# Optimization experiments

Measured on AMD Instinct MI355X. Metric: run time of the kernel, lower is better.

Reference implementation:

```python
import jax, jax.numpy as jnp
import numpy as np

N = 100000
E = 1600000
F_IN = 32
HID = 16


def _sage_conv(x, src, dst, W_l, b_l, W_r):
    # PyG SAGEConv (aggr='mean', normalize=False, root_weight=True):
    #   out = lin_l(mean_{j in N(i)} x_j) + lin_r(x_i)
    # lin_l has bias, lin_r has no bias.
    n = x.shape[0]
    msg_sum = jax.ops.segment_sum(x[src], dst, num_segments=n)          # [N, d]
    deg = jax.ops.segment_sum(jnp.ones_like(dst, dtype=x.dtype), dst, num_segments=n)
    agg = msg_sum / jnp.maximum(deg, 1.0)[:, None]                      # mean, 0 for isolated nodes
    return agg @ W_l.T + b_l + x @ W_r.T


def setup_inputs() -> dict:
    key = jax.random.key(0)
    ks = jax.random.split(key, 8)
    x = jax.random.normal(ks[0], (N, F_IN), dtype=jnp.float32)
    edge_index = jax.random.randint(ks[1], (1, 2, E), 0, N, dtype=jnp.int64)
    s1 = 1.0 / np.sqrt(F_IN)
    s2 = 1.0 / np.sqrt(HID)
    W1_l = jax.random.uniform(ks[2], (HID, F_IN), jnp.float32, -s1, s1)
    b1_l = jax.random.uniform(ks[3], (HID,), jnp.float32, -s1, s1)
    W1_r = jax.random.uniform(ks[4], (HID, F_IN), jnp.float32, -s1, s1)
    W2_l = jax.random.uniform(ks[5], (F_IN, HID), jnp.float32, -s2, s2)
    b2_l = jax.random.uniform(ks[6], (F_IN,), jnp.float32, -s2, s2)
    W2_r = jax.random.uniform(ks[7], (F_IN, HID), jnp.float32, -s2, s2)
    return {"x": x, "edge_index": edge_index, "W1_l": W1_l, "b1_l": b1_l,
            "W1_r": W1_r, "W2_l": W2_l, "b2_l": b2_l, "W2_r": W2_r}


def reference(x, edge_index, W1_l, b1_l, W1_r, W2_l, b2_l, W2_r):
    ei = jnp.squeeze(edge_index, axis=0)  # [2, E]
    src, dst = ei[0], ei[1]
    h = jax.nn.relu(_sage_conv(x, src, dst, W1_l, b1_l, W1_r))
    out = _sage_conv(h, src, dst, W2_l, b2_l, W2_r)
    return out
```

## Files before the change

kernel.cpp:

```cpp
#include <hip/hip_runtime.h>

#define F_IN 32
#define HID 16
#define BSHIFT 6
#define BNODES (1 << BSHIFT)
#define CAP 1440
#define NBINS 2048
#define CHUNK 8192
#define SRCM 0x1FFFFu
#define WS2 17

__device__ __forceinline__ void add4(float4& a, const float4& b) {
    a.x += b.x; a.y += b.y; a.z += b.z; a.w += b.w;
}
__device__ __forceinline__ unsigned pack2(float a, float b) {
    unsigned ua = __float_as_uint(a);
    unsigned ub = __float_as_uint(b);
    ua = (ua + 0x7FFFu + ((ua >> 16) & 1u)) >> 16;
    ub = (ub + 0x7FFFu + ((ub >> 16) & 1u)) >> 16;
    return ua | (ub << 16);
}
__device__ __forceinline__ float lo2f(unsigned u) { return __uint_as_float(u << 16); }
__device__ __forceinline__ float hi2f(unsigned u) { return __uint_as_float(u & 0xFFFF0000u); }
__device__ __forceinline__ float4 unp(uint2 v) {
    return make_float4(lo2f(v.x), hi2f(v.x), lo2f(v.y), hi2f(v.y));
}

__global__ void __launch_bounds__(256) k_pre(const float* __restrict__ x,
                                             const float* __restrict__ W1_l,
                                             const float* __restrict__ b1,
                                             const float* __restrict__ W1_r,
                                             unsigned* __restrict__ y1b,
                                             float* __restrict__ y1r,
                                             const int* __restrict__ ei,
                                             int* __restrict__ bucketCursor,
                                             unsigned* __restrict__ bucketBuf,
                                             int N, int E, int nodeBlocks) {
    __shared__ int cnt[NBINS];
    __shared__ int runBase[NBINS];
    __shared__ float Wa[HID * F_IN];
    __shared__ float Wb[HID * F_IN];
    __shared__ float bb[HID];
    int tid = threadIdx.x;

    if ((int)blockIdx.x < nodeBlocks) {
        for (int i = tid; i < HID * F_IN; i += 256) { Wa[i] = W1_l[i]; Wb[i] = W1_r[i]; }
        if (tid < HID) bb[tid] = b1[tid];
        __syncthreads();
        int node = blockIdx.x * 256 + tid;
        if (node >= N) return;
        float xr[F_IN];
        const float4* xp = (const float4*)(x + (size_t)node * F_IN);
#pragma unroll
        for (int i = 0; i < F_IN / 4; i++) {
            float4 v = xp[i];
            xr[4 * i + 0] = v.x; xr[4 * i + 1] = v.y;
            xr[4 * i + 2] = v.z; xr[4 * i + 3] = v.w;
        }
        float a[HID];
#pragma unroll
        for (int o = 0; o < HID; o++) {
            float s = 0.f;
#pragma unroll
            for (int k = 0; k < F_IN; k++) s += xr[k] * Wa[o * F_IN + k];
            a[o] = s;
        }
        uint4* yp = (uint4*)(y1b + (size_t)node * 8);
        yp[0] = make_uint4(pack2(a[0], a[1]), pack2(a[2], a[3]),
                           pack2(a[4], a[5]), pack2(a[6], a[7]));
        yp[1] = make_uint4(pack2(a[8], a[9]), pack2(a[10], a[11]),
                           pack2(a[12], a[13]), pack2(a[14], a[15]));
#pragma unroll
        for (int o = 0; o < HID; o++) {
            float s = bb[o];
#pragma unroll
            for (int k = 0; k < F_IN; k++) s += xr[k] * Wb[o * F_IN + k];
            a[o] = s;
        }
        float4* rp = (float4*)(y1r + (size_t)node * HID);
        rp[0] = make_float4(a[0], a[1], a[2], a[3]);
        rp[1] = make_float4(a[4], a[5], a[6], a[7]);
        rp[2] = make_float4(a[8], a[9], a[10], a[11]);
        rp[3] = make_float4(a[12], a[13], a[14], a[15]);
        return;
    }

    int pb = blockIdx.x - nodeBlocks;
    int e0 = pb * CHUNK;
    int e1 = min(e0 + CHUNK, E);
    int n4 = (e1 - e0) >> 2;
    const int4* dst4 = (const int4*)(ei + E + e0);
    const int4* src4 = (const int4*)(ei + e0);

#pragma unroll
    for (int i = 0; i < NBINS / 256; i++) cnt[tid + 256 * i] = 0;
    __syncthreads();
    for (int i = tid; i < n4; i += 256) {
        int4 d = dst4[i];
        atomicAdd(&cnt[d.x >> BSHIFT], 1);
        atomicAdd(&cnt[d.y >> BSHIFT], 1);
        atomicAdd(&cnt[d.z >> BSHIFT], 1);
        atomicAdd(&cnt[d.w >> BSHIFT], 1);
    }
    __syncthreads();
#pragma unroll
    for (int i = 0; i < NBINS / 256; i++) {
        int b = tid + 256 * i;
        int c = cnt[b];
        runBase[b] = c ? atomicAdd(&bucketCursor[b], c) : 0;
        cnt[b] = 0;
    }
    __syncthreads();
    for (int i = tid; i < n4; i += 256) {
        int4 d = dst4[i];
        int4 s = src4[i];
        {
            int b = d.x >> BSHIFT;
            int pos = runBase[b] + atomicAdd(&cnt[b], 1);
            if (pos < CAP)
                bucketBuf[(size_t)b * CAP + pos] = ((unsigned)(d.x & (BNODES - 1)) << 17) | (unsigned)s.x;
        }
        {
            int b = d.y >> BSHIFT;
            int pos = runBase[b] + atomicAdd(&cnt[b], 1);
            if (pos < CAP)
                bucketBuf[(size_t)b * CAP + pos] = ((unsigned)(d.y & (BNODES - 1)) << 17) | (unsigned)s.y;
        }
        {
            int b = d.z >> BSHIFT;
            int pos = runBase[b] + atomicAdd(&cnt[b], 1);
            if (pos < CAP)
                bucketBuf[(size_t)b * CAP + pos] = ((unsigned)(d.z & (BNODES - 1)) << 17) | (unsigned)s.z;
        }
        {
            int b = d.w >> BSHIFT;
            int pos = runBase[b] + atomicAdd(&cnt[b], 1);
            if (pos < CAP)
                bucketBuf[(size_t)b * CAP + pos] = ((unsigned)(d.w & (BNODES - 1)) << 17) | (unsigned)s.w;
        }
    }
}

__global__ void __launch_bounds__(256) k_agg1f(const unsigned* __restrict__ y1b,
                                               const float* __restrict__ y1r,
                                               unsigned* __restrict__ bucketBuf,
                                               const int* __restrict__ bucketCursor,
                                               unsigned* __restrict__ hb,
                                               int* __restrict__ meta, int N) {
    __shared__ __align__(16) unsigned sA[CAP];
    __shared__ __align__(16) unsigned sB[CAP];
    __shared__ int hist[BNODES];
    __shared__ int scn[BNODES];
    __shared__ int cur[BNODES];
    int tid = threadIdx.x, b = blockIdx.x;

    if (tid < BNODES) hist[tid] = 0;
    int nRec = min(bucketCursor[b], CAP);
    unsigned* buf = bucketBuf + (size_t)b * CAP;
    int n4s = (nRec + 3) >> 2;
    for (int i = tid; i < n4s; i += 256)
        ((uint4*)sA)[i] = ((const uint4*)buf)[i];
    __syncthreads();
    for (int i = tid; i < nRec; i += 256) atomicAdd(&hist[sA[i] >> 17], 1);
    __syncthreads();
    if (tid < BNODES) scn[tid] = hist[tid];
    __syncthreads();
    for (int off = 1; off < BNODES; off <<= 1) {
        int v = (tid < BNODES && tid >= off) ? scn[tid - off] : 0;
        __syncthreads();
        if (tid < BNODES && tid >= off) scn[tid] += v;
        __syncthreads();
    }
    if (tid < BNODES) cur[tid] = scn[tid] - hist[tid];
    __syncthreads();
    for (int i = tid; i < nRec; i += 256) {
        unsigned r = sA[i];
        int pos = atomicAdd(&cur[r >> 17], 1);
        sB[pos] = r & SRCM;
    }
    __syncthreads();

    for (int i = tid; i < n4s; i += 256)
        ((uint4*)buf)[i] = ((const uint4*)sB)[i];
    if (tid < BNODES) {
        meta[(size_t)b * 128 + tid] = scn[tid] - hist[tid];
        meta[(size_t)b * 128 + BNODES + tid] = scn[tid];
    }

    const uint2* yv = (const uint2*)y1b;
    {
        int nl = tid >> 2, c = tid & 3;
        int node = b * BNODES + nl;
        if (node < N) {
            int start = scn[nl] - hist[nl];
            int dg = hist[nl];
            int jend = start + dg;
            float4 a0 = make_float4(0, 0, 0, 0), a1 = a0;
            int j = start;
            for (; j + 4 <= jend; j += 4) {
                unsigned s0 = sB[j], s1 = sB[j + 1], s2 = sB[j + 2], s3 = sB[j + 3];
                uint2 v0 = yv[(size_t)s0 * 4 + c];
                uint2 v1 = yv[(size_t)s1 * 4 + c];
                uint2 v2 = yv[(size_t)s2 * 4 + c];
                uint2 v3 = yv[(size_t)s3 * 4 + c];
                add4(a0, unp(v0)); add4(a1, unp(v1));
                add4(a0, unp(v2)); add4(a1, unp(v3));
            }
            for (; j < jend; j++) {
                uint2 v = yv[(size_t)sB[j] * 4 + c];
                add4(a0, unp(v));
            }
            add4(a0, a1);
            float inv = 1.0f / (float)(dg > 0 ? dg : 1);
            float4 r4 = ((const float4*)(y1r + (size_t)node * HID))[c];
            float o0 = fmaxf(a0.x * inv + r4.x, 0.0f);
            float o1 = fmaxf(a0.y * inv + r4.y, 0.0f);
            float o2 = fmaxf(a0.z * inv + r4.z, 0.0f);
            float o3 = fmaxf(a0.w * inv + r4.w, 0.0f);
            ((uint2*)hb)[(size_t)node * 4 + c] = make_uint2(pack2(o0, o1), pack2(o2, o3));
        }
    }
}

__global__ void __launch_bounds__(256) k_l2f(const unsigned* __restrict__ hb,
                                             const unsigned* __restrict__ bucketBuf,
                                             const int* __restrict__ bucketCursor,
                                             const int* __restrict__ meta,
                                             const float* __restrict__ W2_l,
                                             const float* __restrict__ b2,
                                             const float* __restrict__ W2_r,
                                             float* __restrict__ out, int N) {
    __shared__ __align__(16) unsigned sB[CAP];
    __shared__ int s0[BNODES];
    __shared__ int s1[BNODES];
    __shared__ float mm[BNODES * (HID + 1)];
    __shared__ float Wl[F_IN * WS2];
    __shared__ float Wr[F_IN * WS2];
    __shared__ float bs[F_IN];
    int tid = threadIdx.x, b = blockIdx.x;

    for (int i = tid; i < F_IN * HID; i += 256) {
        int r = i >> 4, q = i & 15;
        Wl[r * WS2 + q] = W2_l[i];
        Wr[r * WS2 + q] = W2_r[i];
    }
    if (tid < F_IN) bs[tid] = b2[tid];
    if (tid < BNODES) {
        s0[tid] = meta[(size_t)b * 128 + tid];
        s1[tid] = meta[(size_t)b * 128 + BNODES + tid];
    }
    int nRec = min(bucketCursor[b], CAP);
    const uint4* bv = (const uint4*)(bucketBuf + (size_t)b * CAP);
    int n4s = (nRec + 3) >> 2;
    for (int i = tid; i < n4s; i += 256) ((uint4*)sB)[i] = bv[i];
    __syncthreads();

    const uint2* hv = (const uint2*)hb;
    {
        int nl = tid >> 2, c = tid & 3;
        int node = b * BNODES + nl;
        if (node < N) {
            int start = s0[nl];
            int jend = s1[nl];
            int dg = jend - start;
            float4 a0 = make_float4(0, 0, 0, 0), a1 = a0;
            int j = start;
            for (; j + 4 <= jend; j += 4) {
                unsigned v0i = sB[j], v1i = sB[j + 1], v2i = sB[j + 2], v3i = sB[j + 3];
                uint2 v0 = hv[(size_t)v0i * 4 + c];
                uint2 v1 = hv[(size_t)v1i * 4 + c];
                uint2 v2 = hv[(size_t)v2i * 4 + c];
                uint2 v3 = hv[(size_t)v3i * 4 + c];
                add4(a0, unp(v0)); add4(a1, unp(v1));
                add4(a0, unp(v2)); add4(a1, unp(v3));
            }
            for (; j < jend; j++) {
                uint2 v = hv[(size_t)sB[j] * 4 + c];
                add4(a0, unp(v));
            }
            add4(a0, a1);
            float inv = 1.0f / (float)(dg > 0 ? dg : 1);
            mm[nl * (HID + 1) + c * 4 + 0] = a0.x * inv;
            mm[nl * (HID + 1) + c * 4 + 1] = a0.y * inv;
            mm[nl * (HID + 1) + c * 4 + 2] = a0.z * inv;
            mm[nl * (HID + 1) + c * 4 + 3] = a0.w * inv;
        }
    }
    __syncthreads();

    {
        int nl = tid >> 2, c = tid & 3;
        int node = b * BNODES + nl;
        if (node >= N) return;

        float m[HID];
#pragma unroll
        for (int k = 0; k < HID; k++) m[k] = mm[nl * (HID + 1) + k];

        float hr[HID];
        const uint4* hp = (const uint4*)(hb + (size_t)node * 8);
        uint4 u0 = hp[0], u1 = hp[1];
        hr[0] = lo2f(u0.x); hr[1] = hi2f(u0.x); hr[2] = lo2f(u0.y); hr[3] = hi2f(u0.y);
        hr[4] = lo2f(u0.z); hr[5] = hi2f(u0.z); hr[6] = lo2f(u0.w); hr[7] = hi2f(u0.w);
        hr[8] = lo2f(u1.x); hr[9] = hi2f(u1.x); hr[10] = lo2f(u1.y); hr[11] = hi2f(u1.y);
        hr[12] = lo2f(u1.z); hr[13] = hi2f(u1.z); hr[14] = lo2f(u1.w); hr[15] = hi2f(u1.w);

        float a[8];
#pragma unroll
        for (int jj = 0; jj < 8; jj++) {
            int o = c * 8 + jj;
            float s = bs[o];
#pragma unroll
            for (int k = 0; k < HID; k++)
                s += m[k] * Wl[o * WS2 + k] + hr[k] * Wr[o * WS2 + k];
            a[jj] = s;
        }
        float4* op = (float4*)(out + (size_t)node * F_IN + c * 8);
        op[0] = make_float4(a[0], a[1], a[2], a[3]);
        op[1] = make_float4(a[4], a[5], a[6], a[7]);
    }
}

extern "C" void kernel_launch(void* const* d_in, const int* in_sizes, int n_in,
                              void* d_out, int out_size, void* d_ws, size_t ws_size,
                              hipStream_t stream) {
    const float* x    = (const float*)d_in[0];
    const int*   ei   = (const int*)d_in[1];
    const float* W1_l = (const float*)d_in[2];
    const float* b1   = (const float*)d_in[3];
    const float* W1_r = (const float*)d_in[4];
    const float* W2_l = (const float*)d_in[5];
    const float* b2   = (const float*)d_in[6];
    const float* W2_r = (const float*)d_in[7];
    float* out = (float*)d_out;

    const int N = in_sizes[0] / F_IN;
    const int E = in_sizes[1] / 2;
    const int nbuckets = (N + BNODES - 1) >> BSHIFT;

    int* bucketCursor = (int*)d_ws;
    unsigned* bucketBuf = (unsigned*)(bucketCursor + NBINS);
    unsigned* y1b = bucketBuf + (size_t)nbuckets * CAP;
    unsigned* hb  = y1b + (size_t)N * 8;
    int* meta = (int*)(hb + (size_t)N * 8);
    float* y1r = (float*)(meta + (size_t)nbuckets * 128);

    hipMemsetAsync(bucketCursor, 0, NBINS * sizeof(int), stream);

    const int nodeBlocks = (N + 255) / 256;
    const int partBlocks = (E + CHUNK - 1) / CHUNK;

    k_pre<<<nodeBlocks + partBlocks, 256, 0, stream>>>(x, W1_l, b1, W1_r,
                                                       y1b, y1r, ei,
                                                       bucketCursor, bucketBuf,
                                                       N, E, nodeBlocks);
    k_agg1f<<<nbuckets, 256, 0, stream>>>(y1b, y1r, bucketBuf, bucketCursor,
                                          hb, meta, N);
    k_l2f<<<nbuckets, 256, 0, stream>>>(hb, bucketBuf, bucketCursor, meta,
                                        W2_l, b2, W2_r, out, N);
}
```

Before: 147.3 us.

## Replace bucket binning with per-node fixed-capacity adjacency via global atomics

Drops the two-level bucket partition (shared-memory histogram, bucket cursors, then an in-block counting sort in the first aggregation kernel). Each edge now does a global atomicAdd on its destination's degree and writes its source straight into a fixed 64-slot per-node adjacency row. The aggregation kernels then read neighbour lists directly from that row with vectorised loads, so the per-bucket sort and the meta array are gone. In exchange there are 1.6M contended global atomics, scattered 4-byte writes, a larger memset of the degree array, and silently truncated neighbour lists for any node with more than 64 in-edges.

```diff
diff --git a/kernel.cpp b/kernel.cpp
--- a/kernel.cpp
+++ b/kernel.cpp
@@ -2,12 +2,9 @@
 
 #define F_IN 32
 #define HID 16
-#define BSHIFT 6
-#define BNODES (1 << BSHIFT)
-#define CAP 1440
-#define NBINS 2048
-#define CHUNK 8192
-#define SRCM 0x1FFFFu
+#define CAPN 64
+#define CSH 6
+#define CHUNK 4096
 #define WS2 17
 
 __device__ __forceinline__ void add4(float4& a, const float4& b) {
@@ -33,17 +30,15 @@
                                              unsigned* __restrict__ y1b,
                                              float* __restrict__ y1r,
                                              const int* __restrict__ ei,
-                                             int* __restrict__ bucketCursor,
-                                             unsigned* __restrict__ bucketBuf,
+                                             int* __restrict__ deg,
+                                             unsigned* __restrict__ csr,
                                              int N, int E, int nodeBlocks) {
-    __shared__ int cnt[NBINS];
-    __shared__ int runBase[NBINS];
-    __shared__ float Wa[HID * F_IN];
-    __shared__ float Wb[HID * F_IN];
-    __shared__ float bb[HID];
     int tid = threadIdx.x;
 
     if ((int)blockIdx.x < nodeBlocks) {
+        __shared__ float Wa[HID * F_IN];
+        __shared__ float Wb[HID * F_IN];
+        __shared__ float bb[HID];
         for (int i = tid; i < HID * F_IN; i += 256) { Wa[i] = W1_l[i]; Wb[i] = W1_r[i]; }
         if (tid < HID) bb[tid] = b1[tid];
         __syncthreads();
@@ -92,152 +87,72 @@
     const int4* dst4 = (const int4*)(ei + E + e0);
     const int4* src4 = (const int4*)(ei + e0);
 
-#pragma unroll
-    for (int i = 0; i < NBINS / 256; i++) cnt[tid + 256 * i] = 0;
-    __syncthreads();
-    for (int i = tid; i < n4; i += 256) {
-        int4 d = dst4[i];
-        atomicAdd(&cnt[d.x >> BSHIFT], 1);
-        atomicAdd(&cnt[d.y >> BSHIFT], 1);
-        atomicAdd(&cnt[d.z >> BSHIFT], 1);
-        atomicAdd(&cnt[d.w >> BSHIFT], 1);
-    }
-    __syncthreads();
-#pragma unroll
-    for (int i = 0; i < NBINS / 256; i++) {
-        int b = tid + 256 * i;
-        int c = cnt[b];
-        runBase[b] = c ? atomicAdd(&bucketCursor[b], c) : 0;
-        cnt[b] = 0;
-    }
-    __syncthreads();
     for (int i = tid; i < n4; i += 256) {
         int4 d = dst4[i];
         int4 s = src4[i];
-        {
-            int b = d.x >> BSHIFT;
-            int pos = runBase[b] + atomicAdd(&cnt[b], 1);
-            if (pos < CAP)
-                bucketBuf[(size_t)b * CAP + pos] = ((unsigned)(d.x & (BNODES - 1)) << 17) | (unsigned)s.x;
-        }
-        {
-            int b = d.y >> BSHIFT;
-            int pos = runBase[b] + atomicAdd(&cnt[b], 1);
-            if (pos < CAP)
-                bucketBuf[(size_t)b * CAP + pos] = ((unsigned)(d.y & (BNODES - 1)) << 17) | (unsigned)s.y;
-        }
-        {
-            int b = d.z >> BSHIFT;
-            int pos = runBase[b] + atomicAdd(&cnt[b], 1);
-            if (pos < CAP)
-                bucketBuf[(size_t)b * CAP + pos] = ((unsigned)(d.z & (BNODES - 1)) << 17) | (unsigned)s.z;
-        }
-        {
-            int b = d.w >> BSHIFT;
-            int pos = runBase[b] + atomicAdd(&cnt[b], 1);
-            if (pos < CAP)
-                bucketBuf[(size_t)b * CAP + pos] = ((unsigned)(d.w & (BNODES - 1)) << 17) | (unsigned)s.w;
-        }
-    }
-}
-
-__global__ void __launch_bounds__(256) k_agg1f(const unsigned* __restrict__ y1b,
-                                               const float* __restrict__ y1r,
-                                               unsigned* __restrict__ bucketBuf,
-                                               const int* __restrict__ bucketCursor,
-                                               unsigned* __restrict__ hb,
-                                               int* __restrict__ meta, int N) {
-    __shared__ __align__(16) unsigned sA[CAP];
-    __shared__ __align__(16) unsigned sB[CAP];
-    __shared__ int hist[BNODES];
-    __shared__ int scn[BNODES];
-    __shared__ int cur[BNODES];
-    int tid = threadIdx.x, b = blockIdx.x;
-
-    if (tid < BNODES) hist[tid] = 0;
-    int nRec = min(bucketCursor[b], CAP);
-    unsigned* buf = bucketBuf + (size_t)b * CAP;
-    int n4s = (nRec + 3) >> 2;
-    for (int i = tid; i < n4s; i += 256)
-        ((uint4*)sA)[i] = ((const uint4*)buf)[i];
-    __syncthreads();
-    for (int i = tid; i < nRec; i += 256) atomicAdd(&hist[sA[i] >> 17], 1);
-    __syncthreads();
-    if (tid < BNODES) scn[tid] = hist[tid];
-    __syncthreads();
-    for (int off = 1; off < BNODES; off <<= 1) {
-        int v = (tid < BNODES && tid >= off) ? scn[tid - off] : 0;
-        __syncthreads();
-        if (tid < BNODES && tid >= off) scn[tid] += v;
-        __syncthreads();
-    }
-    if (tid < BNODES) cur[tid] = scn[tid] - hist[tid];
-    __syncthreads();
-    for (int i = tid; i < nRec; i += 256) {
-        unsigned r = sA[i];
-        int pos = atomicAdd(&cur[r >> 17], 1);
-        sB[pos] = r & SRCM;
-    }
-    __syncthreads();
-
-    for (int i = tid; i < n4s; i += 256)
-        ((uint4*)buf)[i] = ((const uint4*)sB)[i];
-    if (tid < BNODES) {
-        meta[(size_t)b * 128 + tid] = scn[tid] - hist[tid];
-        meta[(size_t)b * 128 + BNODES + tid] = scn[tid];
-    }
-
+        int p0 = atomicAdd(&deg[d.x], 1);
+        int p1 = atomicAdd(&deg[d.y], 1);
+        int p2 = atomicAdd(&deg[d.z], 1);
+        int p3 = atomicAdd(&deg[d.w], 1);
+        if (p0 < CAPN) csr[((size_t)d.x << CSH) | p0] = (unsigned)s.x;
+        if (p1 < CAPN) csr[((size_t)d.y << CSH) | p1] = (unsigned)s.y;
+        if (p2 < CAPN) csr[((size_t)d.z << CSH) | p2] = (unsigned)s.z;
+        if (p3 < CAPN) csr[((size_t)d.w << CSH) | p3] = (unsigned)s.w;
+    }
+}
+
+__global__ void __launch_bounds__(256) k_agg1(const unsigned* __restrict__ y1b,
+                                              const float* __restrict__ y1r,
+                                              const unsigned* __restrict__ csr,
+                                              const int* __restrict__ deg,
+                                              unsigned* __restrict__ hb, int N) {
+    int tid = threadIdx.x;
+    int nl = tid >> 2, c = tid & 3;
+    int node = blockIdx.x * 64 + nl;
+    if (node >= N) return;
+    int dg = deg[node];
+    int cnt = min(dg, CAPN);
+    const unsigned* cp = csr + ((size_t)node << CSH);
     const uint2* yv = (const uint2*)y1b;
-    {
-        int nl = tid >> 2, c = tid & 3;
-        int node = b * BNODES + nl;
-        if (node < N) {
-            int start = scn[nl] - hist[nl];
-            int dg = hist[nl];
-            int jend = start + dg;
-            float4 a0 = make_float4(0, 0, 0, 0), a1 = a0;
-            int j = start;
-            for (; j + 4 <= jend; j += 4) {
-                unsigned s0 = sB[j], s1 = sB[j + 1], s2 = sB[j + 2], s3 = sB[j + 3];
-                uint2 v0 = yv[(size_t)s0 * 4 + c];
-                uint2 v1 = yv[(size_t)s1 * 4 + c];
-                uint2 v2 = yv[(size_t)s2 * 4 + c];
-                uint2 v3 = yv[(size_t)s3 * 4 + c];
-                add4(a0, unp(v0)); add4(a1, unp(v1));
-                add4(a0, unp(v2)); add4(a1, unp(v3));
-            }
-            for (; j < jend; j++) {
-                uint2 v = yv[(size_t)sB[j] * 4 + c];
-                add4(a0, unp(v));
-            }
-            add4(a0, a1);
-            float inv = 1.0f / (float)(dg > 0 ? dg : 1);
-            float4 r4 = ((const float4*)(y1r + (size_t)node * HID))[c];
-            float o0 = fmaxf(a0.x * inv + r4.x, 0.0f);
-            float o1 = fmaxf(a0.y * inv + r4.y, 0.0f);
-            float o2 = fmaxf(a0.z * inv + r4.z, 0.0f);
-            float o3 = fmaxf(a0.w * inv + r4.w, 0.0f);
-            ((uint2*)hb)[(size_t)node * 4 + c] = make_uint2(pack2(o0, o1), pack2(o2, o3));
-        }
-    }
-}
-
-__global__ void __launch_bounds__(256) k_l2f(const unsigned* __restrict__ hb,
-                                             const unsigned* __restrict__ bucketBuf,
-                                             const int* __restrict__ bucketCursor,
-                                             const int* __restrict__ meta,
-                                             const float* __restrict__ W2_l,
-                                             const float* __restrict__ b2,
-                                             const float* __restrict__ W2_r,
-                                             float* __restrict__ out, int N) {
-    __shared__ __align__(16) unsigned sB[CAP];
-    __shared__ int s0[BNODES];
-    __shared__ int s1[BNODES];
-    __shared__ float mm[BNODES * (HID + 1)];
+    float4 a0 = make_float4(0, 0, 0, 0), a1 = a0;
+    int j = 0;
+    for (; j + 4 <= cnt; j += 4) {
+        uint4 sv = *(const uint4*)(cp + j);
+        uint2 v0 = yv[(size_t)sv.x * 4 + c];
+        uint2 v1 = yv[(size_t)sv.y * 4 + c];
+        uint2 v2 = yv[(size_t)sv.z * 4 + c];
+        uint2 v3 = yv[(size_t)sv.w * 4 + c];
+        add4(a0, unp(v0)); add4(a1, unp(v1));
+        add4(a0, unp(v2)); add4(a1, unp(v3));
+    }
+    for (; j < cnt; j++) {
+        uint2 v = yv[(size_t)cp[j] * 4 + c];
+        add4(a0, unp(v));
+    }
+    add4(a0, a1);
+    float inv = 1.0f / (float)(dg > 0 ? dg : 1);
+    float4 r4 = ((const float4*)(y1r + (size_t)node * HID))[c];
+    float o0 = fmaxf(a0.x * inv + r4.x, 0.0f);
+    float o1 = fmaxf(a0.y * inv + r4.y, 0.0f);
+    float o2 = fmaxf(a0.z * inv + r4.z, 0.0f);
+    float o3 = fmaxf(a0.w * inv + r4.w, 0.0f);
+    ((uint2*)hb)[(size_t)node * 4 + c] = make_uint2(pack2(o0, o1), pack2(o2, o3));
+}
+
+__global__ void __launch_bounds__(256) k_l2(const unsigned* __restrict__ hb,
+                                            const unsigned* __restrict__ csr,
+                                            const int* __restrict__ deg,
+                                            const float* __restrict__ W2_l,
+                                            const float* __restrict__ b2,
+                                            const float* __restrict__ W2_r,
+                                            float* __restrict__ out, int N) {
+    __shared__ float mm[64 * (HID + 1)];
     __shared__ float Wl[F_IN * WS2];
     __shared__ float Wr[F_IN * WS2];
     __shared__ float bs[F_IN];
-    int tid = threadIdx.x, b = blockIdx.x;
+    int tid = threadIdx.x;
+    int nl = tid >> 2, c = tid & 3;
+    int node = blockIdx.x * 64 + nl;
 
     for (int i = tid; i < F_IN * HID; i += 256) {
         int r = i >> 4, q = i & 15;
@@ -245,80 +160,63 @@
         Wr[r * WS2 + q] = W2_r[i];
     }
     if (tid < F_IN) bs[tid] = b2[tid];
-    if (tid < BNODES) {
-        s0[tid] = meta[(size_t)b * 128 + tid];
-        s1[tid] = meta[(size_t)b * 128 + BNODES + tid];
-    }
-    int nRec = min(bucketCursor[b], CAP);
-    const uint4* bv = (const uint4*)(bucketBuf + (size_t)b * CAP);
-    int n4s = (nRec + 3) >> 2;
-    for (int i = tid; i < n4s; i += 256) ((uint4*)sB)[i] = bv[i];
+
+    if (node < N) {
+        int dg = deg[node];
+        int cnt = min(dg, CAPN);
+        const unsigned* cp = csr + ((size_t)node << CSH);
+        const uint2* hv = (const uint2*)hb;
+        float4 a0 = make_float4(0, 0, 0, 0), a1 = a0;
+        int j = 0;
+        for (; j + 4 <= cnt; j += 4) {
+            uint4 sv = *(const uint4*)(cp + j);
+            uint2 v0 = hv[(size_t)sv.x * 4 + c];
+            uint2 v1 = hv[(size_t)sv.y * 4 + c];
+            uint2 v2 = hv[(size_t)sv.z * 4 + c];
+            uint2 v3 = hv[(size_t)sv.w * 4 + c];
+            add4(a0, unp(v0)); add4(a1, unp(v1));
+            add4(a0, unp(v2)); add4(a1, unp(v3));
+        }
+        for (; j < cnt; j++) {
+            uint2 v = hv[(size_t)cp[j] * 4 + c];
+            add4(a0, unp(v));
+        }
+        add4(a0, a1);
+        float inv = 1.0f / (float)(dg > 0 ? dg : 1);
+        mm[nl * (HID + 1) + c * 4 + 0] = a0.x * inv;
+        mm[nl * (HID + 1) + c * 4 + 1] = a0.y * inv;
+        mm[nl * (HID + 1) + c * 4 + 2] = a0.z * inv;
+        mm[nl * (HID + 1) + c * 4 + 3] = a0.w * inv;
+    }
     __syncthreads();
 
-    const uint2* hv = (const uint2*)hb;
-    {
-        int nl = tid >> 2, c = tid & 3;
-        int node = b * BNODES + nl;
-        if (node < N) {
-            int start = s0[nl];
-            int jend = s1[nl];
-            int dg = jend - start;
-            float4 a0 = make_float4(0, 0, 0, 0), a1 = a0;
-            int j = start;
-            for (; j + 4 <= jend; j += 4) {
-                unsigned v0i = sB[j], v1i = sB[j + 1], v2i = sB[j + 2], v3i = sB[j + 3];
-                uint2 v0 = hv[(size_t)v0i * 4 + c];
-                uint2 v1 = hv[(size_t)v1i * 4 + c];
-                uint2 v2 = hv[(size_t)v2i * 4 + c];
-                uint2 v3 = hv[(size_t)v3i * 4 + c];
-                add4(a0, unp(v0)); add4(a1, unp(v1));
-                add4(a0, unp(v2)); add4(a1, unp(v3));
-            }
-            for (; j < jend; j++) {
-                uint2 v = hv[(size_t)sB[j] * 4 + c];
-                add4(a0, unp(v));
-            }
-            add4(a0, a1);
-            float inv = 1.0f / (float)(dg > 0 ? dg : 1);
-            mm[nl * (HID + 1) + c * 4 + 0] = a0.x * inv;
-            mm[nl * (HID + 1) + c * 4 + 1] = a0.y * inv;
-            mm[nl * (HID + 1) + c * 4 + 2] = a0.z * inv;
-            mm[nl * (HID + 1) + c * 4 + 3] = a0.w * inv;
-        }
-    }
-    __syncthreads();
-
-    {
-        int nl = tid >> 2, c = tid & 3;
-        int node = b * BNODES + nl;
-        if (node >= N) return;
-
-        float m[HID];
-#pragma unroll
-        for (int k = 0; k < HID; k++) m[k] = mm[nl * (HID + 1) + k];
-
-        float hr[HID];
-        const uint4* hp = (const uint4*)(hb + (size_t)node * 8);
-        uint4 u0 = hp[0], u1 = hp[1];
-        hr[0] = lo2f(u0.x); hr[1] = hi2f(u0.x); hr[2] = lo2f(u0.y); hr[3] = hi2f(u0.y);
-        hr[4] = lo2f(u0.z); hr[5] = hi2f(u0.z); hr[6] = lo2f(u0.w); hr[7] = hi2f(u0.w);
-        hr[8] = lo2f(u1.x); hr[9] = hi2f(u1.x); hr[10] = lo2f(u1.y); hr[11] = hi2f(u1.y);
-        hr[12] = lo2f(u1.z); hr[13] = hi2f(u1.z); hr[14] = lo2f(u1.w); hr[15] = hi2f(u1.w);
-
-        float a[8];
-#pragma unroll
-        for (int jj = 0; jj < 8; jj++) {
-            int o = c * 8 + jj;
-            float s = bs[o];
-#pragma unroll
-            for (int k = 0; k < HID; k++)
-                s += m[k] * Wl[o * WS2 + k] + hr[k] * Wr[o * WS2 + k];
-            a[jj] = s;
-        }
-        float4* op = (float4*)(out + (size_t)node * F_IN + c * 8);
-        op[0] = make_float4(a[0], a[1], a[2], a[3]);
-        op[1] = make_float4(a[4], a[5], a[6], a[7]);
-    }
+    if (node >= N) return;
+
+    float m[HID];
+#pragma unroll
+    for (int k = 0; k < HID; k++) m[k] = mm[nl * (HID + 1) + k];
+
+    float hr[HID];
+    const uint4* hp = (const uint4*)(hb + (size_t)node * 8);
+    uint4 u0 = hp[0], u1 = hp[1];
+    hr[0] = lo2f(u0.x); hr[1] = hi2f(u0.x); hr[2] = lo2f(u0.y); hr[3] = hi2f(u0.y);
+    hr[4] = lo2f(u0.z); hr[5] = hi2f(u0.z); hr[6] = lo2f(u0.w); hr[7] = hi2f(u0.w);
+    hr[8] = lo2f(u1.x); hr[9] = hi2f(u1.x); hr[10] = lo2f(u1.y); hr[11] = hi2f(u1.y);
+    hr[12] = lo2f(u1.z); hr[13] = hi2f(u1.z); hr[14] = lo2f(u1.w); hr[15] = hi2f(u1.w);
+
+    float a[8];
+#pragma unroll
+    for (int jj = 0; jj < 8; jj++) {
+        int o = c * 8 + jj;
+        float s = bs[o];
+#pragma unroll
+        for (int k = 0; k < HID; k++)
+            s += m[k] * Wl[o * WS2 + k] + hr[k] * Wr[o * WS2 + k];
+        a[jj] = s;
+    }
+    float4* op = (float4*)(out + (size_t)node * F_IN + c * 8);
+    op[0] = make_float4(a[0], a[1], a[2], a[3]);
+    op[1] = make_float4(a[4], a[5], a[6], a[7]);
 }
 
 extern "C" void kernel_launch(void* const* d_in, const int* in_sizes, int n_in,
@@ -336,26 +234,23 @@
 
     const int N = in_sizes[0] / F_IN;
     const int E = in_sizes[1] / 2;
-    const int nbuckets = (N + BNODES - 1) >> BSHIFT;
-
-    int* bucketCursor = (int*)d_ws;
-    unsigned* bucketBuf = (unsigned*)(bucketCursor + NBINS);
-    unsigned* y1b = bucketBuf + (size_t)nbuckets * CAP;
+    const int Npad = (N + 1023) & ~1023;
+
+    int* deg = (int*)d_ws;
+    unsigned* csr = (unsigned*)(deg + Npad);
+    unsigned* y1b = csr + ((size_t)N << CSH);
     unsigned* hb  = y1b + (size_t)N * 8;
-    int* meta = (int*)(hb + (size_t)N * 8);
-    float* y1r = (float*)(meta + (size_t)nbuckets * 128);
-
-    hipMemsetAsync(bucketCursor, 0, NBINS * sizeof(int), stream);
+    float* y1r = (float*)(hb + (size_t)N * 8);
+
+    hipMemsetAsync(deg, 0, Npad * sizeof(int), stream);
 
     const int nodeBlocks = (N + 255) / 256;
     const int partBlocks = (E + CHUNK - 1) / CHUNK;
+    const int aggBlocks  = (N + 63) / 64;
 
     k_pre<<<nodeBlocks + partBlocks, 256, 0, stream>>>(x, W1_l, b1, W1_r,
                                                        y1b, y1r, ei,
-                                                       bucketCursor, bucketBuf,
-                                                       N, E, nodeBlocks);
-    k_agg1f<<<nbuckets, 256, 0, stream>>>(y1b, y1r, bucketBuf, bucketCursor,
-                                          hb, meta, N);
-    k_l2f<<<nbuckets, 256, 0, stream>>>(hb, bucketBuf, bucketCursor, meta,
-                                        W2_l, b2, W2_r, out, N);
-}
+                                                       deg, csr, N, E, nodeBlocks);
+    k_agg1<<<aggBlocks, 256, 0, stream>>>(y1b, y1r, csr, deg, hb, N);
+    k_l2<<<aggBlocks, 256, 0, stream>>>(hb, csr, deg, W2_l, b2, W2_r, out, N);
+}
```

Measured after the change: 231.5 us. 1.57x slower.

## Fuse three kernels into one persistent kernel with software grid barriers

Applied to the files above, without the earlier changes.

Merges the preprocessing/partition, layer-1 aggregation and layer-2 kernels into a single persistent kernel of 768 blocks. Blocks loop over jobs and buckets and are separated by atomic-counter grid barriers. This removes two kernel launch gaps and the tail effects between stages. In exchange, each barrier spins on a global atomic. The fixed grid must be fully co-resident for the barriers to work, otherwise the kernel deadlocks, and the grid-stride loops reduce per-stage parallelism compared with the original launches.

```diff
diff --git a/kernel.cpp b/kernel.cpp
--- a/kernel.cpp
+++ b/kernel.cpp
@@ -9,6 +9,9 @@
 #define CHUNK 8192
 #define SRCM 0x1FFFFu
 #define WS2 17
+#define GRIDN 768
+
+#define SMEM_BYTES 16384
 
 __device__ __forceinline__ void add4(float4& a, const float4& b) {
     a.x += b.x; a.y += b.y; a.z += b.z; a.w += b.w;
@@ -26,298 +29,302 @@
     return make_float4(lo2f(v.x), hi2f(v.x), lo2f(v.y), hi2f(v.y));
 }
 
-__global__ void __launch_bounds__(256) k_pre(const float* __restrict__ x,
-                                             const float* __restrict__ W1_l,
-                                             const float* __restrict__ b1,
-                                             const float* __restrict__ W1_r,
-                                             unsigned* __restrict__ y1b,
-                                             float* __restrict__ y1r,
-                                             const int* __restrict__ ei,
-                                             int* __restrict__ bucketCursor,
-                                             unsigned* __restrict__ bucketBuf,
-                                             int N, int E, int nodeBlocks) {
-    __shared__ int cnt[NBINS];
-    __shared__ int runBase[NBINS];
-    __shared__ float Wa[HID * F_IN];
-    __shared__ float Wb[HID * F_IN];
-    __shared__ float bb[HID];
-    int tid = threadIdx.x;
-
-    if ((int)blockIdx.x < nodeBlocks) {
-        for (int i = tid; i < HID * F_IN; i += 256) { Wa[i] = W1_l[i]; Wb[i] = W1_r[i]; }
-        if (tid < HID) bb[tid] = b1[tid];
-        __syncthreads();
-        int node = blockIdx.x * 256 + tid;
-        if (node >= N) return;
-        float xr[F_IN];
-        const float4* xp = (const float4*)(x + (size_t)node * F_IN);
-#pragma unroll
-        for (int i = 0; i < F_IN / 4; i++) {
-            float4 v = xp[i];
-            xr[4 * i + 0] = v.x; xr[4 * i + 1] = v.y;
-            xr[4 * i + 2] = v.z; xr[4 * i + 3] = v.w;
-        }
-        float a[HID];
-#pragma unroll
-        for (int o = 0; o < HID; o++) {
-            float s = 0.f;
-#pragma unroll
-            for (int k = 0; k < F_IN; k++) s += xr[k] * Wa[o * F_IN + k];
-            a[o] = s;
-        }
-        uint4* yp = (uint4*)(y1b + (size_t)node * 8);
-        yp[0] = make_uint4(pack2(a[0], a[1]), pack2(a[2], a[3]),
-                           pack2(a[4], a[5]), pack2(a[6], a[7]));
-        yp[1] = make_uint4(pack2(a[8], a[9]), pack2(a[10], a[11]),
-                           pack2(a[12], a[13]), pack2(a[14], a[15]));
-#pragma unroll
-        for (int o = 0; o < HID; o++) {
-            float s = bb[o];
-#pragma unroll
-            for (int k = 0; k < F_IN; k++) s += xr[k] * Wb[o * F_IN + k];
-            a[o] = s;
-        }
-        float4* rp = (float4*)(y1r + (size_t)node * HID);
-        rp[0] = make_float4(a[0], a[1], a[2], a[3]);
-        rp[1] = make_float4(a[4], a[5], a[6], a[7]);
-        rp[2] = make_float4(a[8], a[9], a[10], a[11]);
-        rp[3] = make_float4(a[12], a[13], a[14], a[15]);
-        return;
-    }
-
-    int pb = blockIdx.x - nodeBlocks;
-    int e0 = pb * CHUNK;
-    int e1 = min(e0 + CHUNK, E);
-    int n4 = (e1 - e0) >> 2;
-    const int4* dst4 = (const int4*)(ei + E + e0);
-    const int4* src4 = (const int4*)(ei + e0);
-
-#pragma unroll
-    for (int i = 0; i < NBINS / 256; i++) cnt[tid + 256 * i] = 0;
+__device__ __forceinline__ void gbar(int* cnt, int target) {
+    __threadfence();
     __syncthreads();
-    for (int i = tid; i < n4; i += 256) {
-        int4 d = dst4[i];
-        atomicAdd(&cnt[d.x >> BSHIFT], 1);
-        atomicAdd(&cnt[d.y >> BSHIFT], 1);
-        atomicAdd(&cnt[d.z >> BSHIFT], 1);
-        atomicAdd(&cnt[d.w >> BSHIFT], 1);
+    if (threadIdx.x == 0) {
+        atomicAdd(cnt, 1);
+        while (__hip_atomic_load(cnt, __ATOMIC_RELAXED, __HIP_MEMORY_SCOPE_AGENT) < target)
+            __builtin_amdgcn_s_sleep(32);
     }
     __syncthreads();
-#pragma unroll
-    for (int i = 0; i < NBINS / 256; i++) {
-        int b = tid + 256 * i;
-        int c = cnt[b];
-        runBase[b] = c ? atomicAdd(&bucketCursor[b], c) : 0;
-        cnt[b] = 0;
+    __threadfence();
+}
+
+__global__ void __launch_bounds__(256, 4)
+k_mega(const float* __restrict__ x, const float* __restrict__ W1_l,
+       const float* __restrict__ b1, const float* __restrict__ W1_r,
+       const float* __restrict__ W2_l, const float* __restrict__ b2,
+       const float* __restrict__ W2_r, const int* __restrict__ ei,
+       int* __restrict__ gsync, int* __restrict__ bucketCursor,
+       unsigned* __restrict__ bucketBuf, unsigned* __restrict__ y1b,
+       float* __restrict__ y1r, unsigned* __restrict__ hb,
+       int* __restrict__ meta, float* __restrict__ out,
+       int N, int E, int nodeBlocks, int partBlocks, int nbuckets) {
+    __shared__ __align__(16) unsigned char smem[SMEM_BYTES];
+    int tid = threadIdx.x;
+    int bid = blockIdx.x;
+    int nG = gridDim.x;
+
+    for (int job = bid; job < nodeBlocks + partBlocks; job += nG) {
+        if (job < nodeBlocks) {
+            float* Wa = (float*)smem;
+            float* Wb = (float*)(smem + 2048);
+            float* bb = (float*)(smem + 4096);
+            for (int i = tid; i < HID * F_IN; i += 256) { Wa[i] = W1_l[i]; Wb[i] = W1_r[i]; }
+            if (tid < HID) bb[tid] = b1[tid];
+            __syncthreads();
+            int node = job * 256 + tid;
+            if (node < N) {
+                float xr[F_IN];
+                const float4* xp = (const float4*)(x + (size_t)node * F_IN);
+#pragma unroll
+                for (int i = 0; i < F_IN / 4; i++) {
+                    float4 v = xp[i];
+                    xr[4 * i + 0] = v.x; xr[4 * i + 1] = v.y;
+                    xr[4 * i + 2] = v.z; xr[4 * i + 3] = v.w;
+                }
+                float a[HID];
+#pragma unroll
+                for (int o = 0; o < HID; o++) {
+                    float s = 0.f;
+#pragma unroll
+                    for (int k = 0; k < F_IN; k++) s += xr[k] * Wa[o * F_IN + k];
+                    a[o] = s;
+                }
+                uint4* yp = (uint4*)(y1b + (size_t)node * 8);
+                yp[0] = make_uint4(pack2(a[0], a[1]), pack2(a[2], a[3]),
+                                   pack2(a[4], a[5]), pack2(a[6], a[7]));
+                yp[1] = make_uint4(pack2(a[8], a[9]), pack2(a[10], a[11]),
+                                   pack2(a[12], a[13]), pack2(a[14], a[15]));
+#pragma unroll
+                for (int o = 0; o < HID; o++) {
+                    float s = bb[o];
+#pragma unroll
+                    for (int k = 0; k < F_IN; k++) s += xr[k] * Wb[o * F_IN + k];
+                    a[o] = s;
+                }
+                float4* rp = (float4*)(y1r + (size_t)node * HID);
+                rp[0] = make_float4(a[0], a[1], a[2], a[3]);
+                rp[1] = make_float4(a[4], a[5], a[6], a[7]);
+                rp[2] = make_float4(a[8], a[9], a[10], a[11]);
+                rp[3] = make_float4(a[12], a[13], a[14], a[15]);
+            }
+        } else {
+            int* cnt = (int*)smem;
+            int* runBase = (int*)(smem + 8192);
+            int pb = job - nodeBlocks;
+            int e0 = pb * CHUNK;
+            int e1 = min(e0 + CHUNK, E);
+            int n4 = (e1 - e0) >> 2;
+            const int4* dst4 = (const int4*)(ei + E + e0);
+            const int4* src4 = (const int4*)(ei + e0);
+
+#pragma unroll
+            for (int i = 0; i < NBINS / 256; i++) cnt[tid + 256 * i] = 0;
+            __syncthreads();
+            for (int i = tid; i < n4; i += 256) {
+                int4 d = dst4[i];
+                atomicAdd(&cnt[d.x >> BSHIFT], 1);
+                atomicAdd(&cnt[d.y >> BSHIFT], 1);
+                atomicAdd(&cnt[d.z >> BSHIFT], 1);
+                atomicAdd(&cnt[d.w >> BSHIFT], 1);
+            }
+            __syncthreads();
+#pragma unroll
+            for (int i = 0; i < NBINS / 256; i++) {
+                int b = tid + 256 * i;
+                int c = cnt[b];
+                runBase[b] = c ? atomicAdd(&bucketCursor[b], c) : 0;
+                cnt[b] = 0;
+            }
+            __syncthreads();
+            for (int i = tid; i < n4; i += 256) {
+                int4 d = dst4[i];
+                int4 s = src4[i];
+                {
+                    int b = d.x >> BSHIFT;
+                    int pos = runBase[b] + atomicAdd(&cnt[b], 1);
+                    if (pos < CAP)
+                        bucketBuf[(size_t)b * CAP + pos] = ((unsigned)(d.x & (BNODES - 1)) << 17) | (unsigned)s.x;
+                }
+                {
+                    int b = d.y >> BSHIFT;
+                    int pos = runBase[b] + atomicAdd(&cnt[b], 1);
+                    if (pos < CAP)
+                        bucketBuf[(size_t)b * CAP + pos] = ((unsigned)(d.y & (BNODES - 1)) << 17) | (unsigned)s.y;
+                }
+                {
+                    int b = d.z >> BSHIFT;
+                    int pos = runBase[b] + atomicAdd(&cnt[b], 1);
+                    if (pos < CAP)
+                        bucketBuf[(size_t)b * CAP + pos] = ((unsigned)(d.z & (BNODES - 1)) << 17) | (unsigned)s.z;
+                }
+                {
+                    int b = d.w >> BSHIFT;
+                    int pos = runBase[b] + atomicAdd(&cnt[b], 1);
+                    if (pos < CAP)
+                        bucketBuf[(size_t)b * CAP + pos] = ((unsigned)(d.w & (BNODES - 1)) << 17) | (unsigned)s.w;
+                }
+            }
+        }
+        __syncthreads();
     }
-    __syncthreads();
-    for (int i = tid; i < n4; i += 256) {
-        int4 d = dst4[i];
-        int4 s = src4[i];
-        {
-            int b = d.x >> BSHIFT;
-            int pos = runBase[b] + atomicAdd(&cnt[b], 1);
-            if (pos < CAP)
-                bucketBuf[(size_t)b * CAP + pos] = ((unsigned)(d.x & (BNODES - 1)) << 17) | (unsigned)s.x;
-        }
-        {
-            int b = d.y >> BSHIFT;
-            int pos = runBase[b] + atomicAdd(&cnt[b], 1);
-            if (pos < CAP)
-                bucketBuf[(size_t)b * CAP + pos] = ((unsigned)(d.y & (BNODES - 1)) << 17) | (unsigned)s.y;
-        }
-        {
-            int b = d.z >> BSHIFT;
-            int pos = runBase[b] + atomicAdd(&cnt[b], 1);
-            if (pos < CAP)
-                bucketBuf[(size_t)b * CAP + pos] = ((unsigned)(d.z & (BNODES - 1)) << 17) | (unsigned)s.z;
-        }
-        {
-            int b = d.w >> BSHIFT;
-            int pos = runBase[b] + atomicAdd(&cnt[b], 1);
-            if (pos < CAP)
-                bucketBuf[(size_t)b * CAP + pos] = ((unsigned)(d.w & (BNODES - 1)) << 17) | (unsigned)s.w;
+    gbar(gsync, nG);
+
+    {
+        unsigned* sA = (unsigned*)smem;
+        unsigned* sB = (unsigned*)(smem + 5760);
+        int* hist = (int*)(smem + 11520);
+        int* scn  = (int*)(smem + 11776);
+        int* cur  = (int*)(smem + 12032);
+        for (int b = bid; b < nbuckets; b += nG) {
+            if (tid < BNODES) hist[tid] = 0;
+            int nRec = min(bucketCursor[b], CAP);
+            unsigned* buf = bucketBuf + (size_t)b * CAP;
+            int n4s = (nRec + 3) >> 2;
+            for (int i = tid; i < n4s; i += 256)
+                ((uint4*)sA)[i] = ((const uint4*)buf)[i];
+            __syncthreads();
+            for (int i = tid; i < nRec; i += 256) atomicAdd(&hist[sA[i] >> 17], 1);
+            __syncthreads();
+            if (tid < BNODES) scn[tid] = hist[tid];
+            __syncthreads();
+            for (int off = 1; off < BNODES; off <<= 1) {
+                int v = (tid < BNODES && tid >= off) ? scn[tid - off] : 0;
+                __syncthreads();
+                if (tid < BNODES && tid >= off) scn[tid] += v;
+                __syncthreads();
+            }
+            if (tid < BNODES) cur[tid] = scn[tid] - hist[tid];
+            __syncthreads();
+            for (int i = tid; i < nRec; i += 256) {
+                unsigned r = sA[i];
+                int pos = atomicAdd(&cur[r >> 17], 1);
+                sB[pos] = r & SRCM;
+            }
+            __syncthreads();
+
+            for (int i = tid; i < n4s; i += 256)
+                ((uint4*)buf)[i] = ((const uint4*)sB)[i];
+            if (tid < BNODES) {
+                meta[(size_t)b * 128 + tid] = scn[tid] - hist[tid];
+                meta[(size_t)b * 128 + BNODES + tid] = scn[tid];
+            }
+
+            const uint2* yv = (const uint2*)y1b;
+            {
+                int nl = tid >> 2, c = tid & 3;
+                int node = b * BNODES + nl;
+                if (node < N) {
+                    int start = scn[nl] - hist[nl];
+                    int dg = hist[nl];
+                    int jend = start + dg;
+                    float4 a0 = make_float4(0, 0, 0, 0), a1 = a0;
+                    int j = start;
+                    for (; j + 4 <= jend; j += 4) {
+                        unsigned s0 = sB[j], s1 = sB[j + 1], s2 = sB[j + 2], s3 = sB[j + 3];
+                        uint2 v0 = yv[(size_t)s0 * 4 + c];
+                        uint2 v1 = yv[(size_t)s1 * 4 + c];
+                        uint2 v2 = yv[(size_t)s2 * 4 + c];
+                        uint2 v3 = yv[(size_t)s3 * 4 + c];
+                        add4(a0, unp(v0)); add4(a1, unp(v1));
+                        add4(a0, unp(v2)); add4(a1, unp(v3));
+                    }
+                    for (; j < jend; j++) {
+                        uint2 v = yv[(size_t)sB[j] * 4 + c];
+                        add4(a0, unp(v));
+                    }
+                    add4(a0, a1);
+                    float inv = 1.0f / (float)(dg > 0 ? dg : 1);
+                    float4 r4 = ((const float4*)(y1r + (size_t)node * HID))[c];
+                    float o0 = fmaxf(a0.x * inv + r4.x, 0.0f);
+                    float o1 = fmaxf(a0.y * inv + r4.y, 0.0f);
+                    float o2 = fmaxf(a0.z * inv + r4.z, 0.0f);
+                    float o3 = fmaxf(a0.w * inv + r4.w, 0.0f);
+                    ((uint2*)hb)[(size_t)node * 4 + c] = make_uint2(pack2(o0, o1), pack2(o2, o3));
+                }
+            }
+            __syncthreads();
         }
     }
-}
-
-__global__ void __launch_bounds__(256) k_agg1f(const unsigned* __restrict__ y1b,
-                                               const float* __restrict__ y1r,
-                                               unsigned* __restrict__ bucketBuf,
-                                               const int* __restrict__ bucketCursor,
-                                               unsigned* __restrict__ hb,
-                                               int* __restrict__ meta, int N) {
-    __shared__ __align__(16) unsigned sA[CAP];
-    __shared__ __align__(16) unsigned sB[CAP];
-    __shared__ int hist[BNODES];
-    __shared__ int scn[BNODES];
-    __shared__ int cur[BNODES];
-    int tid = threadIdx.x, b = blockIdx.x;
-
-    if (tid < BNODES) hist[tid] = 0;
-    int nRec = min(bucketCursor[b], CAP);
-    unsigned* buf = bucketBuf + (size_t)b * CAP;
-    int n4s = (nRec + 3) >> 2;
-    for (int i = tid; i < n4s; i += 256)
-        ((uint4*)sA)[i] = ((const uint4*)buf)[i];
-    __syncthreads();
-    for (int i = tid; i < nRec; i += 256) atomicAdd(&hist[sA[i] >> 17], 1);
-    __syncthreads();
-    if (tid < BNODES) scn[tid] = hist[tid];
-    __syncthreads();
-    for (int off = 1; off < BNODES; off <<= 1) {
-        int v = (tid < BNODES && tid >= off) ? scn[tid - off] : 0;
-        __syncthreads();
-        if (tid < BNODES && tid >= off) scn[tid] += v;
-        __syncthreads();
-    }
-    if (tid < BNODES) cur[tid] = scn[tid] - hist[tid];
-    __syncthreads();
-    for (int i = tid; i < nRec; i += 256) {
-        unsigned r = sA[i];
-        int pos = atomicAdd(&cur[r >> 17], 1);
-        sB[pos] = r & SRCM;
-    }
-    __syncthreads();
-
-    for (int i = tid; i < n4s; i += 256)
-        ((uint4*)buf)[i] = ((const uint4*)sB)[i];
-    if (tid < BNODES) {
-        meta[(size_t)b * 128 + tid] = scn[tid] - hist[tid];
-        meta[(size_t)b * 128 + BNODES + tid] = scn[tid];
-    }
-
-    const uint2* yv = (const uint2*)y1b;
+    gbar(gsync, 2 * nG);
+
     {
-        int nl = tid >> 2, c = tid & 3;
-        int node = b * BNODES + nl;
-        if (node < N) {
-            int start = scn[nl] - hist[nl];
-            int dg = hist[nl];
-            int jend = start + dg;
-            float4 a0 = make_float4(0, 0, 0, 0), a1 = a0;
-            int j = start;
-            for (; j + 4 <= jend; j += 4) {
-                unsigned s0 = sB[j], s1 = sB[j + 1], s2 = sB[j + 2], s3 = sB[j + 3];
-                uint2 v0 = yv[(size_t)s0 * 4 + c];
-                uint2 v1 = yv[(size_t)s1 * 4 + c];
-                uint2 v2 = yv[(size_t)s2 * 4 + c];
-                uint2 v3 = yv[(size_t)s3 * 4 + c];
-                add4(a0, unp(v0)); add4(a1, unp(v1));
-                add4(a0, unp(v2)); add4(a1, unp(v3));
-            }
-            for (; j < jend; j++) {
-                uint2 v = yv[(size_t)sB[j] * 4 + c];
-                add4(a0, unp(v));
-            }
-            add4(a0, a1);
-            float inv = 1.0f / (float)(dg > 0 ? dg : 1);
-            float4 r4 = ((const float4*)(y1r + (size_t)node * HID))[c];
-            float o0 = fmaxf(a0.x * inv + r4.x, 0.0f);
-            float o1 = fmaxf(a0.y * inv + r4.y, 0.0f);
-            float o2 = fmaxf(a0.z * inv + r4.z, 0.0f);
-            float o3 = fmaxf(a0.w * inv + r4.w, 0.0f);
-            ((uint2*)hb)[(size_t)node * 4 + c] = make_uint2(pack2(o0, o1), pack2(o2, o3));
+        unsigned* sL = (unsigned*)smem;
+        int* s0a = (int*)(smem + 5760);
+        int* s1a = (int*)(smem + 6016);
+        float* mm = (float*)(smem + 6272);
+        float* Wl = (float*)(smem + 10624);
+        float* Wr = (float*)(smem + 12800);
+        float* bs = (float*)(smem + 14976);
+        for (int i = tid; i < F_IN * HID; i += 256) {
+            int r = i >> 4, q = i & 15;
+            Wl[r * WS2 + q] = W2_l[i];
+            Wr[r * WS2 + q] = W2_r[i];
         }
-    }
-}
-
-__global__ void __launch_bounds__(256) k_l2f(const unsigned* __restrict__ hb,
-                                             const unsigned* __restrict__ bucketBuf,
-                                             const int* __restrict__ bucketCursor,
-                                             const int* __restrict__ meta,
-                                             const float* __restrict__ W2_l,
-                                             const float* __restrict__ b2,
-                                             const float* __restrict__ W2_r,
-                                             float* __restrict__ out, int N) {
-    __shared__ __align__(16) unsigned sB[CAP];
-    __shared__ int s0[BNODES];
-    __shared__ int s1[BNODES];
-    __shared__ float mm[BNODES * (HID + 1)];
-    __shared__ float Wl[F_IN * WS2];
-    __shared__ float Wr[F_IN * WS2];
-    __shared__ float bs[F_IN];
-    int tid = threadIdx.x, b = blockIdx.x;
-
-    for (int i = tid; i < F_IN * HID; i += 256) {
-        int r = i >> 4, q = i & 15;
-        Wl[r * WS2 + q] = W2_l[i];
-        Wr[r * WS2 + q] = W2_r[i];
-    }
-    if (tid < F_IN) bs[tid] = b2[tid];
-    if (tid < BNODES) {
-        s0[tid] = meta[(size_t)b * 128 + tid];
-        s1[tid] = meta[(size_t)b * 128 + BNODES + tid];
-    }
-    int nRec = min(bucketCursor[b], CAP);
-    const uint4* bv = (const uint4*)(bucketBuf + (size_t)b * CAP);
-    int n4s = (nRec + 3) >> 2;
-    for (int i = tid; i < n4s; i += 256) ((uint4*)sB)[i] = bv[i];
-    __syncthreads();
-
-    const uint2* hv = (const uint2*)hb;
-    {
-        int nl = tid >> 2, c = tid & 3;
-        int node = b * BNODES + nl;
-        if (node < N) {
-            int start = s0[nl];
-            int jend = s1[nl];
-            int dg = jend - start;
-            float4 a0 = make_float4(0, 0, 0, 0), a1 = a0;
-            int j = start;
-            for (; j + 4 <= jend; j += 4) {
-                unsigned v0i = sB[j], v1i = sB[j + 1], v2i = sB[j + 2], v3i = sB[j + 3];
-                uint2 v0 = hv[(size_t)v0i * 4 + c];
-                uint2 v1 = hv[(size_t)v1i * 4 + c];
-                uint2 v2 = hv[(size_t)v2i * 4 + c];
-                uint2 v3 = hv[(size_t)v3i * 4 + c];
-                add4(a0, unp(v0)); add4(a1, unp(v1));
-                add4(a0, unp(v2)); add4(a1, unp(v3));
-            }
-            for (; j < jend; j++) {
-                uint2 v = hv[(size_t)sB[j] * 4 + c];
-                add4(a0, unp(v));
-            }
-            add4(a0, a1);
-            float inv = 1.0f / (float)(dg > 0 ? dg : 1);
-            mm[nl * (HID + 1) + c * 4 + 0] = a0.x * inv;
-            mm[nl * (HID + 1) + c * 4 + 1] = a0.y * inv;
-            mm[nl * (HID + 1) + c * 4 + 2] = a0.z * inv;
-            mm[nl * (HID + 1) + c * 4 + 3] = a0.w * inv;
+        if (tid < F_IN) bs[tid] = b2[tid];
+        for (int b = bid; b < nbuckets; b += nG) {
+            if (tid < BNODES) {
+                s0a[tid] = meta[(size_t)b * 128 + tid];
+                s1a[tid] = meta[(size_t)b * 128 + BNODES + tid];
+            }
+            int nRec = min(bucketCursor[b], CAP);
+            const uint4* bv = (const uint4*)(bucketBuf + (size_t)b * CAP);
+            int n4s = (nRec + 3) >> 2;
+            for (int i = tid; i < n4s; i += 256) ((uint4*)sL)[i] = bv[i];
+            __syncthreads();
+
+            int nl = tid >> 2, c = tid & 3;
+            int node = b * BNODES + nl;
+            const uint2* hv = (const uint2*)hb;
+            if (node < N) {
+                int start = s0a[nl];
+                int jend = s1a[nl];
+                int dg = jend - start;
+                float4 a0 = make_float4(0, 0, 0, 0), a1 = a0;
+                int j = start;
+                for (; j + 4 <= jend; j += 4) {
+                    unsigned v0i = sL[j], v1i = sL[j + 1], v2i = sL[j + 2], v3i = sL[j + 3];
+                    uint2 v0 = hv[(size_t)v0i * 4 + c];
+                    uint2 v1 = hv[(size_t)v1i * 4 + c];
+                    uint2 v2 = hv[(size_t)v2i * 4 + c];
+                    uint2 v3 = hv[(size_t)v3i * 4 + c];
+                    add4(a0, unp(v0)); add4(a1, unp(v1));
+                    add4(a0, unp(v2)); add4(a1, unp(v3));
+                }
+                for (; j < jend; j++) {
+                    uint2 v = hv[(size_t)sL[j] * 4 + c];
+                    add4(a0, unp(v));
+                }
+                add4(a0, a1);
+                float inv = 1.0f / (float)(dg > 0 ? dg : 1);
+                mm[nl * (HID + 1) + c * 4 + 0] = a0.x * inv;
+                mm[nl * (HID + 1) + c * 4 + 1] = a0.y * inv;
+                mm[nl * (HID + 1) + c * 4 + 2] = a0.z * inv;
+                mm[nl * (HID + 1) + c * 4 + 3] = a0.w * inv;
+            }
+            __syncthreads();
+
+            if (node < N) {
+                float m[HID];
+#pragma unroll
+                for (int k = 0; k < HID; k++) m[k] = mm[nl * (HID + 1) + k];
+
+                float hr[HID];
+                const uint4* hp = (const uint4*)(hb + (size_t)node * 8);
+                uint4 u0 = hp[0], u1 = hp[1];
+                hr[0] = lo2f(u0.x); hr[1] = hi2f(u0.x); hr[2] = lo2f(u0.y); hr[3] = hi2f(u0.y);
+                hr[4] = lo2f(u0.z); hr[5] = hi2f(u0.z); hr[6] = lo2f(u0.w); hr[7] = hi2f(u0.w);
+                hr[8] = lo2f(u1.x); hr[9] = hi2f(u1.x); hr[10] = lo2f(u1.y); hr[11] = hi2f(u1.y);
+                hr[12] = lo2f(u1.z); hr[13] = hi2f(u1.z); hr[14] = lo2f(u1.w); hr[15] = hi2f(u1.w);
+
+                float a[8];
+#pragma unroll
+                for (int jj = 0; jj < 8; jj++) {
+                    int o = c * 8 + jj;
+                    float s = bs[o];
+#pragma unroll
+                    for (int k = 0; k < HID; k++)
+                        s += m[k] * Wl[o * WS2 + k] + hr[k] * Wr[o * WS2 + k];
+                    a[jj] = s;
+                }
+                float4* op = (float4*)(out + (size_t)node * F_IN + c * 8);
+                op[0] = make_float4(a[0], a[1], a[2], a[3]);
+                op[1] = make_float4(a[4], a[5], a[6], a[7]);
+            }
+            __syncthreads();
         }
-    }
-    __syncthreads();
-
-    {
-        int nl = tid >> 2, c = tid & 3;
-        int node = b * BNODES + nl;
-        if (node >= N) return;
-
-        float m[HID];
-#pragma unroll
-        for (int k = 0; k < HID; k++) m[k] = mm[nl * (HID + 1) + k];
-
-        float hr[HID];
-        const uint4* hp = (const uint4*)(hb + (size_t)node * 8);
-        uint4 u0 = hp[0], u1 = hp[1];
-        hr[0] = lo2f(u0.x); hr[1] = hi2f(u0.x); hr[2] = lo2f(u0.y); hr[3] = hi2f(u0.y);
-        hr[4] = lo2f(u0.z); hr[5] = hi2f(u0.z); hr[6] = lo2f(u0.w); hr[7] = hi2f(u0.w);
-        hr[8] = lo2f(u1.x); hr[9] = hi2f(u1.x); hr[10] = lo2f(u1.y); hr[11] = hi2f(u1.y);
-        hr[12] = lo2f(u1.z); hr[13] = hi2f(u1.z); hr[14] = lo2f(u1.w); hr[15] = hi2f(u1.w);
-
-        float a[8];
-#pragma unroll
-        for (int jj = 0; jj < 8; jj++) {
-            int o = c * 8 + jj;
-            float s = bs[o];
-#pragma unroll
-            for (int k = 0; k < HID; k++)
-                s += m[k] * Wl[o * WS2 + k] + hr[k] * Wr[o * WS2 + k];
-            a[jj] = s;
-        }
-        float4* op = (float4*)(out + (size_t)node * F_IN + c * 8);
-        op[0] = make_float4(a[0], a[1], a[2], a[3]);
-        op[1] = make_float4(a[4], a[5], a[6], a[7]);
     }
 }
 
@@ -338,24 +345,21 @@
     const int E = in_sizes[1] / 2;
     const int nbuckets = (N + BNODES - 1) >> BSHIFT;
 
-    int* bucketCursor = (int*)d_ws;
+    int* gsync = (int*)d_ws;
+    int* bucketCursor = gsync + 16;
     unsigned* bucketBuf = (unsigned*)(bucketCursor + NBINS);
     unsigned* y1b = bucketBuf + (size_t)nbuckets * CAP;
     unsigned* hb  = y1b + (size_t)N * 8;
     int* meta = (int*)(hb + (size_t)N * 8);
     float* y1r = (float*)(meta + (size_t)nbuckets * 128);
 
-    hipMemsetAsync(bucketCursor, 0, NBINS * sizeof(int), stream);
+    hipMemsetAsync(gsync, 0, (16 + NBINS) * sizeof(int), stream);
 
     const int nodeBlocks = (N + 255) / 256;
     const int partBlocks = (E + CHUNK - 1) / CHUNK;
 
-    k_pre<<<nodeBlocks + partBlocks, 256, 0, stream>>>(x, W1_l, b1, W1_r,
-                                                       y1b, y1r, ei,
-                                                       bucketCursor, bucketBuf,
-                                                       N, E, nodeBlocks);
-    k_agg1f<<<nbuckets, 256, 0, stream>>>(y1b, y1r, bucketBuf, bucketCursor,
-                                          hb, meta, N);
-    k_l2f<<<nbuckets, 256, 0, stream>>>(hb, bucketBuf, bucketCursor, meta,
-                                        W2_l, b2, W2_r, out, N);
-}
+    k_mega<<<GRIDN, 256, 0, stream>>>(x, W1_l, b1, W1_r, W2_l, b2, W2_r, ei,
+                                      gsync, bucketCursor, bucketBuf, y1b,
+                                      y1r, hb, meta, out,
+                                      N, E, nodeBlocks, partBlocks, nbuckets);
+}
```

Measured after the change: 483.1 us. +227.9%, slower.
